# Kernel optimization log

Hardware: AMD Instinct MI355X
Metric: run time of the kernel (lower is better)

Reference implementation:

```python
import jax, jax.numpy as jnp
import numpy as np

VOCAB, EMBED, HIDDEN = 50000, 256, 512
BATCH, SEQ = 64, 512


def setup_inputs() -> dict:
    key = jax.random.key(0)
    ks = jax.random.split(key, 20)
    s = 0.05  # small init scale to keep gates out of saturation
    inp = {
        "tokens": jax.random.randint(ks[0], (BATCH, SEQ), 0, VOCAB, dtype=jnp.int64),
        "emb": jax.random.normal(ks[1], (VOCAB, EMBED), jnp.float32) * s,
        "W1f": jax.random.normal(ks[2], (EMBED, 4 * HIDDEN), jnp.float32) * s,
        "U1f": jax.random.normal(ks[3], (HIDDEN, 4 * HIDDEN), jnp.float32) * s,
        "b1f": jax.random.normal(ks[4], (4 * HIDDEN,), jnp.float32) * s,
        "W2f": jax.random.normal(ks[5], (HIDDEN, 4 * HIDDEN), jnp.float32) * s,
        "U2f": jax.random.normal(ks[6], (HIDDEN, 4 * HIDDEN), jnp.float32) * s,
        "b2f": jax.random.normal(ks[7], (4 * HIDDEN,), jnp.float32) * s,
        "W1b": jax.random.normal(ks[8], (EMBED, 4 * HIDDEN), jnp.float32) * s,
        "U1b": jax.random.normal(ks[9], (HIDDEN, 4 * HIDDEN), jnp.float32) * s,
        "b1b": jax.random.normal(ks[10], (4 * HIDDEN,), jnp.float32) * s,
        "W2b": jax.random.normal(ks[11], (HIDDEN, 4 * HIDDEN), jnp.float32) * s,
        "U2b": jax.random.normal(ks[12], (HIDDEN, 4 * HIDDEN), jnp.float32) * s,
        "b2b": jax.random.normal(ks[13], (4 * HIDDEN,), jnp.float32) * s,
        "Wd": jax.random.normal(ks[14], (2 * HIDDEN, 5), jnp.float32) * s,
        "bd": jax.random.normal(ks[15], (5,), jnp.float32) * s,
    }
    return inp


def _lstm_cell(x, h, c, W, U, b):
    # Keras gate order: i, f, g (candidate), o
    z = x @ W + h @ U + b
    i, f, g, o = jnp.split(z, 4, axis=-1)
    c = jax.nn.sigmoid(f) * c + jax.nn.sigmoid(i) * jnp.tanh(g)
    h = jax.nn.sigmoid(o) * jnp.tanh(c)
    return h, c


def _run_stack(xs, W1, U1, b1, W2, U2, b2):
    # xs: [T, B, E]; stacked 2-layer LSTM, return last hidden of layer 2: [B, H]
    B = xs.shape[1]
    H = U1.shape[0]
    init = tuple(jnp.zeros((B, H), xs.dtype) for _ in range(4))

    def step(carry, x_t):
        h1, c1, h2, c2 = carry
        h1, c1 = _lstm_cell(x_t, h1, c1, W1, U1, b1)
        h2, c2 = _lstm_cell(h1, h2, c2, W2, U2, b2)
        return (h1, c1, h2, c2), None

    (h1, c1, h2, c2), _ = jax.lax.scan(step, init, xs)
    return h2


def reference(tokens, emb, W1f, U1f, b1f, W2f, U2f, b2f,
              W1b, U1b, b1b, W2b, U2b, b2b, Wd, bd):
    x = emb[tokens]                 # [B, T, E]
    xs = jnp.swapaxes(x, 0, 1)      # [T, B, E]
    h_fwd = _run_stack(xs, W1f, U1f, b1f, W2f, U2f, b2f)          # [B, H]
    h_bwd = _run_stack(xs[::-1], W1b, U1b, b1b, W2b, U2b, b2b)    # [B, H]
    feat = jnp.concatenate([h_fwd, h_bwd], axis=-1)               # [B, 2H]
    return feat @ Wd + bd                                         # [B, 5]
```

## Files before the change

### kernel.cpp

```cpp
#include <hip/hip_runtime.h>
#include <hip/hip_bf16.h>

#define TSEQ 512
#define NB   64
#define NE   256
#define NH   512
#define NG   2048

static const size_t OFF_W1  = 0;
static const size_t OFF_W2  = 6291456;
static const size_t OFF_X   = 14680064;
static const size_t OFF_H1  = 31457280;
static const size_t OFF_H2  = 31981568;
static const size_t OFF_HF  = 32505856;
static const size_t OFF_CNT = 32636928;

typedef __bf16 v8bf __attribute__((ext_vector_type(8)));
typedef float  v4f  __attribute__((ext_vector_type(4)));

#define MFMA16(a_, b_, c_) __builtin_amdgcn_mfma_f32_16x16x32_bf16((a_), (b_), (c_), 0, 0, 0)

static __device__ __forceinline__ v8bf load_h8(const __bf16* p) {
    unsigned long long lo = __hip_atomic_load((unsigned long long*)p,     __ATOMIC_RELAXED, __HIP_MEMORY_SCOPE_AGENT);
    unsigned long long hi = __hip_atomic_load((unsigned long long*)p + 1, __ATOMIC_RELAXED, __HIP_MEMORY_SCOPE_AGENT);
    union { unsigned long long q[2]; v8bf v; } u;
    u.q[0] = lo; u.q[1] = hi;
    return u.v;
}

static __device__ __forceinline__ unsigned short bf16_bits(float f) {
    __bf16 b = (__bf16)f;
    return __builtin_bit_cast(unsigned short, b);
}

__global__ void wconv_kernel(const float* __restrict__ Wf, const float* __restrict__ Uf,
                             const float* __restrict__ Wb, const float* __restrict__ Ub,
                             char* __restrict__ dst, int NC, int KX)
{
    int id = blockIdx.x * 256 + threadIdx.x;
    int j    = id & 7;
    int lane = (id >> 3) & 63;
    int t    = (id >> 9) & 1;
    int rest = id >> 10;
    int c    = rest % NC;
    int ds   = rest / NC;
    int slice = ds & 63;
    int dirr  = ds >> 6;
    int coll = t * 16 + (lane & 15);
    int k    = c * 32 + (lane >> 4) * 8 + j;
    int gate = coll >> 3, jjj = coll & 7;
    int zcol = gate * 512 + slice * 8 + jjj;
    const float* W = dirr ? Wb : Wf;
    const float* U = dirr ? Ub : Uf;
    float v = (k < KX) ? W[(size_t)k * NG + zcol] : U[(size_t)(k - KX) * NG + zcol];
    ((__bf16*)dst)[id] = (__bf16)v;
}

__global__ void gather_x_kernel(const int* __restrict__ tokens, const float* __restrict__ emb,
                                char* __restrict__ ws)
{
    size_t id = (size_t)blockIdx.x * 256 + threadIdx.x;
    int j  = (int)(id & 7);
    int m  = (int)((id >> 3) & 63);
    int kb = (int)((id >> 9) & 31);
    int t  = (int)(id >> 14);
    int tok = tokens[m * TSEQ + t];
    float v = emb[(size_t)tok * NE + kb * 8 + j];
    ((__bf16*)(ws + OFF_X))[(size_t)t * 16384 + (kb * 64 + m) * 8 + j] = (__bf16)v;
    if (id < 16384) ((int*)(ws + OFF_CNT))[id] = 0;
}

template<int LAYER>
__device__ void run_layer(char* __restrict__ ws, const char* __restrict__ smem,
                          int dir, int slice, int tid,
                          const float* __restrict__ bb)
{
    const int lane = tid & 63;
    const int wv   = tid >> 6;
    const int colc = lane & 15;
    const int q    = lane >> 4;
    const int m0   = wv * 16;
    const int jj   = colc & 7;
    const int hcol = slice * 8 + jj;

    __bf16* h1ring = (__bf16*)(ws + OFF_H1 + (size_t)dir * (4 * 65536));
    __bf16* h2ring = (__bf16*)(ws + OFF_H2 + (size_t)dir * (4 * 65536));
    const char* Xfrag = ws + OFF_X;
    __bf16* hfin = (__bf16*)(ws + OFF_HF) + (size_t)dir * (NB * NH);

    int* T = (int*)(ws + OFF_CNT);
    const int rep = ((slice << 2) | wv) & 15;
    int* p1   = T + (dir * 2 + 0) * 4096 + rep * 256 + wv * 64 + lane;
    int* p2   = T + (dir * 2 + 1) * 4096 + rep * 256 + wv * 64 + lane;
    int* ownb = T + (dir * 2 + LAYER) * 4096;

    const float bi  = bb[hcol];
    const float bf_ = bb[512 + hcol];
    const float bg  = bb[1024 + hcol];
    const float bo  = bb[1536 + hcol];

    float cst[4] = {0.f, 0.f, 0.f, 0.f};

    const int aoff = (m0 + colc) * 8;

    #pragma unroll 1
    for (int s = 0; s < TSEQ; ++s) {
        v4f acc0a = {0,0,0,0}, acc1a = {0,0,0,0};
        v4f acc0b = {0,0,0,0}, acc1b = {0,0,0,0};

        if (LAYER == 0) {
            const int xs = dir ? (TSEQ - 1 - s) : s;
            const char* xb = Xfrag + (size_t)xs * 32768;
            #pragma unroll
            for (int c = 0; c < 8; ++c) {
                v8bf a  = *(const v8bf*)(xb + (((4 * c + q) * 64 + m0 + colc) * 16));
                v8bf w0 = *(const v8bf*)(smem + (c * 2 + 0) * 1024 + lane * 16);
                v8bf w1 = *(const v8bf*)(smem + (c * 2 + 1) * 1024 + lane * 16);
                if (c & 1) { acc0b = MFMA16(a, w0, acc0b); acc1b = MFMA16(a, w1, acc1b); }
                else       { acc0a = MFMA16(a, w0, acc0a); acc1a = MFMA16(a, w1, acc1a); }
            }
        }

        {
            const int t1 = LAYER ? s + 1 : s;
            const int t2 = LAYER ? s : s - 3;
            if (t1 > 0) {
                while (true) {
                    int v1 = __hip_atomic_load(p1, __ATOMIC_RELAXED, __HIP_MEMORY_SCOPE_AGENT);
                    bool ok = (v1 >= t1);
                    if (t2 > 0) {
                        int v2 = __hip_atomic_load(p2, __ATOMIC_RELAXED, __HIP_MEMORY_SCOPE_AGENT);
                        ok = ok && (v2 >= t2);
                    }
                    if (__all(ok)) break;
                }
            }
        }

        if (LAYER == 0) {
            if (s > 0) {
                const __bf16* hb = h1ring + (size_t)((s - 1) & 3) * 32768;
                v8bf ah[16];
                #pragma unroll
                for (int c = 0; c < 16; ++c)
                    ah[c] = load_h8(hb + (4 * c + q) * 512 + aoff);
                __builtin_amdgcn_sched_barrier(0);
                #pragma unroll
                for (int c = 0; c < 16; ++c) {
                    v8bf w0 = *(const v8bf*)(smem + ((8 + c) * 2 + 0) * 1024 + lane * 16);
                    v8bf w1 = *(const v8bf*)(smem + ((8 + c) * 2 + 1) * 1024 + lane * 16);
                    if (c & 1) { acc0b = MFMA16(ah[c], w0, acc0b); acc1b = MFMA16(ah[c], w1, acc1b); }
                    else       { acc0a = MFMA16(ah[c], w0, acc0a); acc1a = MFMA16(ah[c], w1, acc1a); }
                }
            }
        } else {
            const __bf16* hb1 = h1ring + (size_t)(s & 3) * 32768;
            v8bf a0[16], a1[16];
            #pragma unroll
            for (int c = 0; c < 16; ++c)
                a0[c] = load_h8(hb1 + (4 * c + q) * 512 + aoff);
            if (s > 0) {
                const __bf16* hb2 = h2ring + (size_t)((s - 1) & 3) * 32768;
                #pragma unroll
                for (int c = 0; c < 16; ++c)
                    a1[c] = load_h8(hb2 + (4 * c + q) * 512 + aoff);
            }
            __builtin_amdgcn_sched_barrier(0);
            #pragma unroll
            for (int c = 0; c < 16; ++c) {
                v8bf w0 = *(const v8bf*)(smem + (c * 2 + 0) * 1024 + lane * 16);
                v8bf w1 = *(const v8bf*)(smem + (c * 2 + 1) * 1024 + lane * 16);
                if (c & 1) { acc0b = MFMA16(a0[c], w0, acc0b); acc1b = MFMA16(a0[c], w1, acc1b); }
                else       { acc0a = MFMA16(a0[c], w0, acc0a); acc1a = MFMA16(a0[c], w1, acc1a); }
            }
            if (s > 0) {
                #pragma unroll
                for (int c = 0; c < 16; ++c) {
                    v8bf w0 = *(const v8bf*)(smem + ((16 + c) * 2 + 0) * 1024 + lane * 16);
                    v8bf w1 = *(const v8bf*)(smem + ((16 + c) * 2 + 1) * 1024 + lane * 16);
                    if (c & 1) { acc0b = MFMA16(a1[c], w0, acc0b); acc1b = MFMA16(a1[c], w1, acc1b); }
                    else       { acc0a = MFMA16(a1[c], w0, acc0a); acc1a = MFMA16(a1[c], w1, acc1a); }
                }
            }
        }

        v4f z0 = acc0a + acc0b;
        v4f z1 = acc1a + acc1b;

        float hv[4];
        #pragma unroll
        for (int r = 0; r < 4; ++r) {
            float p0 = __shfl_xor(z0[r], 8, 64);
            float p1 = __shfl_xor(z1[r], 8, 64);
            float zi, zf, zg, zo;
            if (colc < 8) { zi = z0[r]; zf = p0;    zg = z1[r]; zo = p1;    }
            else          { zi = p0;    zf = z0[r]; zg = p1;    zo = z1[r]; }
            zi += bi; zf += bf_; zg += bg; zo += bo;
            float gi = 1.f / (1.f + __expf(-zi));
            float gf = 1.f / (1.f + __expf(-zf));
            float gg = 1.f - 2.f / (1.f + __expf(2.f * zg));
            float go = 1.f / (1.f + __expf(-zo));
            float cn = gf * cst[r] + gi * gg;
            cst[r] = cn;
            float th = 1.f - 2.f / (1.f + __expf(2.f * cn));
            hv[r] = go * th;
        }

        __bf16* hd = (LAYER ? h2ring : h1ring) + (size_t)(s & 3) * 32768;
        {
            unsigned u0, u1, u2, u3;
            {
                float pv0 = __shfl_xor(hv[0], 1, 64);
                float pv1 = __shfl_xor(hv[1], 1, 64);
                float pv2 = __shfl_xor(hv[2], 1, 64);
                float pv3 = __shfl_xor(hv[3], 1, 64);
                u0 = (unsigned)bf16_bits(hv[0]) | ((unsigned)bf16_bits(pv0) << 16);
                u1 = (unsigned)bf16_bits(hv[1]) | ((unsigned)bf16_bits(pv1) << 16);
                u2 = (unsigned)bf16_bits(hv[2]) | ((unsigned)bf16_bits(pv2) << 16);
                u3 = (unsigned)bf16_bits(hv[3]) | ((unsigned)bf16_bits(pv3) << 16);
            }
            const bool sel1 = (colc & 2) != 0;
            const bool sel2 = (colc & 4) != 0;
            unsigned t;
            t = __shfl_xor(sel1 ? u0 : u1, 2, 64); if (sel1) u0 = t; else u1 = t;
            t = __shfl_xor(sel1 ? u2 : u3, 2, 64); if (sel1) u2 = t; else u3 = t;
            t = __shfl_xor(sel2 ? u0 : u2, 4, 64); if (sel2) u0 = t; else u2 = t;
            t = __shfl_xor(sel2 ? u1 : u3, 4, 64); if (sel2) u1 = t; else u3 = t;
            if (((colc & 1) == 0) && (colc < 8)) {
                const int m = m0 + q * 4 + (colc >> 1);
                unsigned long long lo = (unsigned long long)u0 | ((unsigned long long)u1 << 32);
                unsigned long long hi = (unsigned long long)u2 | ((unsigned long long)u3 << 32);
                unsigned long long* dp = (unsigned long long*)(hd + (slice * 64 + m) * 8);
                __hip_atomic_store(dp,     lo, __ATOMIC_RELAXED, __HIP_MEMORY_SCOPE_AGENT);
                __hip_atomic_store(dp + 1, hi, __ATOMIC_RELAXED, __HIP_MEMORY_SCOPE_AGENT);
            }
        }
        if (LAYER == 1 && s == TSEQ - 1 && colc < 8) {
            #pragma unroll
            for (int r = 0; r < 4; ++r)
                hfin[(size_t)(m0 + q * 4 + r) * NH + hcol] = (__bf16)hv[r];
        }

        asm volatile("s_waitcnt vmcnt(0)" ::: "memory");
        if (lane < 16)
            __hip_atomic_store(ownb + lane * 256 + wv * 64 + slice, s + 1,
                               __ATOMIC_RELAXED, __HIP_MEMORY_SCOPE_AGENT);
    }
}

__global__ __launch_bounds__(256, 1) void lstm_persist(
    char* __restrict__ ws,
    const float* __restrict__ b1f, const float* __restrict__ b2f,
    const float* __restrict__ b1b, const float* __restrict__ b2b)
{
    const int tid   = threadIdx.x;
    const int bid   = blockIdx.x;
    const int dir   = bid >> 7;
    const int layer = (bid >> 6) & 1;
    const int slice = bid & 63;

    const int NC = layer ? 32 : 24;
    const int wbytes = NC * 2048;

    __shared__ char smem[65536];
    {
        const char* wsrc = ws + (layer ? OFF_W2 : OFF_W1)
                         + (size_t)(dir * 64 + slice) * (size_t)wbytes;
        for (int i = tid * 16; i < wbytes; i += 256 * 16)
            *(uint4*)(smem + i) = *(const uint4*)(wsrc + i);
    }
    __syncthreads();

    const float* bb = layer ? (dir ? b2b : b2f) : (dir ? b1b : b1f);
    if (layer == 0) run_layer<0>(ws, smem, dir, slice, tid, bb);
    else            run_layer<1>(ws, smem, dir, slice, tid, bb);
}

__global__ void head_kernel(const char* __restrict__ ws, const float* __restrict__ Wd,
                            const float* __restrict__ bd, float* __restrict__ out)
{
    int b = blockIdx.x;
    int lane = threadIdx.x;
    const __bf16* hfF = (const __bf16*)(ws + OFF_HF) + (size_t)b * NH;
    const __bf16* hfB = (const __bf16*)(ws + OFF_HF) + (size_t)(NB * NH) + (size_t)b * NH;
    #pragma unroll
    for (int o = 0; o < 5; ++o) {
        float sum = 0.f;
        for (int k = lane; k < 2 * NH; k += 64) {
            float fv = (k < NH) ? (float)hfF[k] : (float)hfB[k - NH];
            sum += fv * Wd[(size_t)k * 5 + o];
        }
        #pragma unroll
        for (int off = 32; off > 0; off >>= 1) sum += __shfl_down(sum, off, 64);
        if (lane == 0) out[b * 5 + o] = sum + bd[o];
    }
}

extern "C" void kernel_launch(void* const* d_in, const int* in_sizes, int n_in,
                              void* d_out, int out_size, void* d_ws, size_t ws_size,
                              hipStream_t stream)
{
    const int*   tokens = (const int*)  d_in[0];
    const float* emb    = (const float*)d_in[1];
    const float* W1f    = (const float*)d_in[2];
    const float* U1f    = (const float*)d_in[3];
    const float* b1f    = (const float*)d_in[4];
    const float* W2f    = (const float*)d_in[5];
    const float* U2f    = (const float*)d_in[6];
    const float* b2f    = (const float*)d_in[7];
    const float* W1b    = (const float*)d_in[8];
    const float* U1b    = (const float*)d_in[9];
    const float* b1b    = (const float*)d_in[10];
    const float* W2b    = (const float*)d_in[11];
    const float* U2b    = (const float*)d_in[12];
    const float* b2b    = (const float*)d_in[13];
    const float* Wd     = (const float*)d_in[14];
    const float* bd     = (const float*)d_in[15];
    char* ws = (char*)d_ws;

    wconv_kernel<<<12288, 256, 0, stream>>>(W1f, U1f, W1b, U1b, ws + OFF_W1, 24, 256);
    wconv_kernel<<<16384, 256, 0, stream>>>(W2f, U2f, W2b, U2b, ws + OFF_W2, 32, 512);
    gather_x_kernel<<<32768, 256, 0, stream>>>(tokens, emb, ws);
    lstm_persist<<<256, 256, 0, stream>>>(ws, b1f, b2f, b1b, b2b);
    head_kernel<<<NB, 64, 0, stream>>>(ws, Wd, bd, (float*)d_out);
}
```

Measured before the change: 3.510 ms.

## Replace layer-1 ready counters with parity-tagged h data and speculative prefetch

Removes the per-step counter polling between producers and consumers of the h1/h2 rings. Each stored bf16 value now carries a parity bit (bit 14) that flips every four steps, and consumers re-load until every fragment shows the expected parity. h values are clamped so that bit is never set by real data. Next-step h fragments are issued right after the store so loads overlap the barrier latency, and only the layer-0 backpressure counter remains. This trades a small precision loss (one exponent bit repurposed, clamp to ±0.996) and possible repeated reloads for fewer atomic round trips on the serial critical path.

```diff
diff --git a/kernel.cpp b/kernel.cpp
--- a/kernel.cpp
+++ b/kernel.cpp
@@ -20,9 +20,12 @@
 
 #define MFMA16(a_, b_, c_) __builtin_amdgcn_mfma_f32_16x16x32_bf16((a_), (b_), (c_), 0, 0, 0)
 
+#define AG_LOAD(p)     __hip_atomic_load((p), __ATOMIC_RELAXED, __HIP_MEMORY_SCOPE_AGENT)
+#define AG_STORE(p, v) __hip_atomic_store((p), (v), __ATOMIC_RELAXED, __HIP_MEMORY_SCOPE_AGENT)
+
 static __device__ __forceinline__ v8bf load_h8(const __bf16* p) {
-    unsigned long long lo = __hip_atomic_load((unsigned long long*)p,     __ATOMIC_RELAXED, __HIP_MEMORY_SCOPE_AGENT);
-    unsigned long long hi = __hip_atomic_load((unsigned long long*)p + 1, __ATOMIC_RELAXED, __HIP_MEMORY_SCOPE_AGENT);
+    unsigned long long lo = AG_LOAD((unsigned long long*)p);
+    unsigned long long hi = AG_LOAD((unsigned long long*)p + 1);
     union { unsigned long long q[2]; v8bf v; } u;
     u.q[0] = lo; u.q[1] = hi;
     return u.v;
@@ -32,6 +35,39 @@
     __bf16 b = (__bf16)f;
     return __builtin_bit_cast(unsigned short, b);
 }
+
+static __device__ __forceinline__ unsigned frag_chk_clr(v8bf* f, unsigned pm) {
+    union { v8bf v; unsigned u[4]; } a; a.v = *f;
+    unsigned bad = ((a.u[0] ^ pm) | (a.u[1] ^ pm) | (a.u[2] ^ pm) | (a.u[3] ^ pm)) & 0x40004000u;
+    a.u[0] &= 0xBFFFBFFFu; a.u[1] &= 0xBFFFBFFFu;
+    a.u[2] &= 0xBFFFBFFFu; a.u[3] &= 0xBFFFBFFFu;
+    *f = a.v;
+    return bad;
+}
+
+#define ISSUE16(sp_, base_)                                                    \
+    {                                                                          \
+        const __bf16* _b = (base_);                                            \
+        _Pragma("unroll")                                                      \
+        for (int c = 0; c < 16; ++c)                                           \
+            sp_[c] = load_h8(_b + (4 * c + q) * 512 + aoff);                   \
+    }
+
+#define VALIDATE16(sp_, base_, pm_)                                            \
+    {                                                                          \
+        const __bf16* _b = (base_);                                            \
+        const unsigned _pm = (pm_);                                            \
+        while (true) {                                                         \
+            unsigned _bad = 0u;                                                \
+            _Pragma("unroll")                                                  \
+            for (int c = 0; c < 16; ++c) _bad |= frag_chk_clr(&sp_[c], _pm);   \
+            if (__all(_bad == 0u)) break;                                      \
+            _Pragma("unroll")                                                  \
+            for (int c = 0; c < 16; ++c)                                       \
+                sp_[c] = load_h8(_b + (4 * c + q) * 512 + aoff);               \
+            __builtin_amdgcn_sched_barrier(0);                                 \
+        }                                                                      \
+    }
 
 __global__ void wconv_kernel(const float* __restrict__ Wf, const float* __restrict__ Uf,
                              const float* __restrict__ Wb, const float* __restrict__ Ub,
@@ -67,7 +103,8 @@
     int tok = tokens[m * TSEQ + t];
     float v = emb[(size_t)tok * NE + kb * 8 + j];
     ((__bf16*)(ws + OFF_X))[(size_t)t * 16384 + (kb * 64 + m) * 8 + j] = (__bf16)v;
-    if (id < 16384) ((int*)(ws + OFF_CNT))[id] = 0;
+    if (id < 262144) ((unsigned*)(ws + OFF_H1))[id] = 0x40004000u;
+    if (id < 16384)  ((int*)(ws + OFF_CNT))[id] = 0;
 }
 
 template<int LAYER>
@@ -90,9 +127,8 @@
 
     int* T = (int*)(ws + OFF_CNT);
     const int rep = ((slice << 2) | wv) & 15;
-    int* p1   = T + (dir * 2 + 0) * 4096 + rep * 256 + wv * 64 + lane;
-    int* p2   = T + (dir * 2 + 1) * 4096 + rep * 256 + wv * 64 + lane;
-    int* ownb = T + (dir * 2 + LAYER) * 4096;
+    int* p2   = T + dir * 4096 + rep * 256 + wv * 64 + lane;
+    int* ownb = T + dir * 4096;
 
     const float bi  = bb[hcol];
     const float bf_ = bb[512 + hcol];
@@ -100,13 +136,22 @@
     const float bo  = bb[1536 + hcol];
 
     float cst[4] = {0.f, 0.f, 0.f, 0.f};
-
     const int aoff = (m0 + colc) * 8;
+
+    v8bf sp0[16];
+    v8bf sp1[16];
+
+    if (LAYER == 1) { ISSUE16(sp0, h1ring); }
 
     #pragma unroll 1
     for (int s = 0; s < TSEQ; ++s) {
+        const unsigned pmC = ((s >> 2) & 1)       ? 0x40004000u : 0u;
+        const unsigned pmP = (((s - 1) >> 2) & 1) ? 0x40004000u : 0u;
+
         v4f acc0a = {0,0,0,0}, acc1a = {0,0,0,0};
         v4f acc0b = {0,0,0,0}, acc1b = {0,0,0,0};
+
+        int gvG = (LAYER == 0 && s > 3) ? AG_LOAD(p2) : 0x7fffffff;
 
         if (LAYER == 0) {
             const int xs = dir ? (TSEQ - 1 - s) : s;
@@ -119,67 +164,36 @@
                 if (c & 1) { acc0b = MFMA16(a, w0, acc0b); acc1b = MFMA16(a, w1, acc1b); }
                 else       { acc0a = MFMA16(a, w0, acc0a); acc1a = MFMA16(a, w1, acc1a); }
             }
-        }
-
-        {
-            const int t1 = LAYER ? s + 1 : s;
-            const int t2 = LAYER ? s : s - 3;
-            if (t1 > 0) {
-                while (true) {
-                    int v1 = __hip_atomic_load(p1, __ATOMIC_RELAXED, __HIP_MEMORY_SCOPE_AGENT);
-                    bool ok = (v1 >= t1);
-                    if (t2 > 0) {
-                        int v2 = __hip_atomic_load(p2, __ATOMIC_RELAXED, __HIP_MEMORY_SCOPE_AGENT);
-                        ok = ok && (v2 >= t2);
-                    }
-                    if (__all(ok)) break;
-                }
-            }
-        }
-
-        if (LAYER == 0) {
             if (s > 0) {
-                const __bf16* hb = h1ring + (size_t)((s - 1) & 3) * 32768;
-                v8bf ah[16];
-                #pragma unroll
-                for (int c = 0; c < 16; ++c)
-                    ah[c] = load_h8(hb + (4 * c + q) * 512 + aoff);
+                VALIDATE16(sp0, h1ring + (size_t)((s - 1) & 3) * 32768, pmP);
                 __builtin_amdgcn_sched_barrier(0);
                 #pragma unroll
                 for (int c = 0; c < 16; ++c) {
                     v8bf w0 = *(const v8bf*)(smem + ((8 + c) * 2 + 0) * 1024 + lane * 16);
                     v8bf w1 = *(const v8bf*)(smem + ((8 + c) * 2 + 1) * 1024 + lane * 16);
-                    if (c & 1) { acc0b = MFMA16(ah[c], w0, acc0b); acc1b = MFMA16(ah[c], w1, acc1b); }
-                    else       { acc0a = MFMA16(ah[c], w0, acc0a); acc1a = MFMA16(ah[c], w1, acc1a); }
+                    if (c & 1) { acc0b = MFMA16(sp0[c], w0, acc0b); acc1b = MFMA16(sp0[c], w1, acc1b); }
+                    else       { acc0a = MFMA16(sp0[c], w0, acc0a); acc1a = MFMA16(sp0[c], w1, acc1a); }
                 }
             }
         } else {
-            const __bf16* hb1 = h1ring + (size_t)(s & 3) * 32768;
-            v8bf a0[16], a1[16];
-            #pragma unroll
-            for (int c = 0; c < 16; ++c)
-                a0[c] = load_h8(hb1 + (4 * c + q) * 512 + aoff);
-            if (s > 0) {
-                const __bf16* hb2 = h2ring + (size_t)((s - 1) & 3) * 32768;
-                #pragma unroll
-                for (int c = 0; c < 16; ++c)
-                    a1[c] = load_h8(hb2 + (4 * c + q) * 512 + aoff);
-            }
+            VALIDATE16(sp0, h1ring + (size_t)(s & 3) * 32768, pmC);
             __builtin_amdgcn_sched_barrier(0);
             #pragma unroll
             for (int c = 0; c < 16; ++c) {
                 v8bf w0 = *(const v8bf*)(smem + (c * 2 + 0) * 1024 + lane * 16);
                 v8bf w1 = *(const v8bf*)(smem + (c * 2 + 1) * 1024 + lane * 16);
-                if (c & 1) { acc0b = MFMA16(a0[c], w0, acc0b); acc1b = MFMA16(a0[c], w1, acc1b); }
-                else       { acc0a = MFMA16(a0[c], w0, acc0a); acc1a = MFMA16(a0[c], w1, acc1a); }
+                if (c & 1) { acc0b = MFMA16(sp0[c], w0, acc0b); acc1b = MFMA16(sp0[c], w1, acc1b); }
+                else       { acc0a = MFMA16(sp0[c], w0, acc0a); acc1a = MFMA16(sp0[c], w1, acc1a); }
             }
             if (s > 0) {
+                VALIDATE16(sp1, h2ring + (size_t)((s - 1) & 3) * 32768, pmP);
+                __builtin_amdgcn_sched_barrier(0);
                 #pragma unroll
                 for (int c = 0; c < 16; ++c) {
                     v8bf w0 = *(const v8bf*)(smem + ((16 + c) * 2 + 0) * 1024 + lane * 16);
                     v8bf w1 = *(const v8bf*)(smem + ((16 + c) * 2 + 1) * 1024 + lane * 16);
-                    if (c & 1) { acc0b = MFMA16(a1[c], w0, acc0b); acc1b = MFMA16(a1[c], w1, acc1b); }
-                    else       { acc0a = MFMA16(a1[c], w0, acc0a); acc1a = MFMA16(a1[c], w1, acc1a); }
+                    if (c & 1) { acc0b = MFMA16(sp1[c], w0, acc0b); acc1b = MFMA16(sp1[c], w1, acc1b); }
+                    else       { acc0a = MFMA16(sp1[c], w0, acc0a); acc1a = MFMA16(sp1[c], w1, acc1a); }
                 }
             }
         }
@@ -203,7 +217,14 @@
             float cn = gf * cst[r] + gi * gg;
             cst[r] = cn;
             float th = 1.f - 2.f / (1.f + __expf(2.f * cn));
-            hv[r] = go * th;
+            hv[r] = fminf(fmaxf(go * th, -0.99609375f), 0.99609375f);
+        }
+
+        if (LAYER == 0 && s > 3 && !__all(gvG >= s - 3)) {
+            while (true) {
+                int v2 = AG_LOAD(p2);
+                if (__all(v2 >= s - 3)) break;
+            }
         }
 
         __bf16* hd = (LAYER ? h2ring : h1ring) + (size_t)(s & 3) * 32768;
@@ -228,11 +249,12 @@
             t = __shfl_xor(sel2 ? u1 : u3, 4, 64); if (sel2) u1 = t; else u3 = t;
             if (((colc & 1) == 0) && (colc < 8)) {
                 const int m = m0 + q * 4 + (colc >> 1);
-                unsigned long long lo = (unsigned long long)u0 | ((unsigned long long)u1 << 32);
-                unsigned long long hi = (unsigned long long)u2 | ((unsigned long long)u3 << 32);
+                const unsigned long long pm64 = pmC ? 0x4000400040004000ULL : 0ULL;
+                unsigned long long lo = ((unsigned long long)u0 | ((unsigned long long)u1 << 32)) | pm64;
+                unsigned long long hi = ((unsigned long long)u2 | ((unsigned long long)u3 << 32)) | pm64;
                 unsigned long long* dp = (unsigned long long*)(hd + (slice * 64 + m) * 8);
-                __hip_atomic_store(dp,     lo, __ATOMIC_RELAXED, __HIP_MEMORY_SCOPE_AGENT);
-                __hip_atomic_store(dp + 1, hi, __ATOMIC_RELAXED, __HIP_MEMORY_SCOPE_AGENT);
+                AG_STORE(dp,     lo);
+                AG_STORE(dp + 1, hi);
             }
         }
         if (LAYER == 1 && s == TSEQ - 1 && colc < 8) {
@@ -241,10 +263,19 @@
                 hfin[(size_t)(m0 + q * 4 + r) * NH + hcol] = (__bf16)hv[r];
         }
 
-        asm volatile("s_waitcnt vmcnt(0)" ::: "memory");
-        if (lane < 16)
-            __hip_atomic_store(ownb + lane * 256 + wv * 64 + slice, s + 1,
-                               __ATOMIC_RELAXED, __HIP_MEMORY_SCOPE_AGENT);
+        if (LAYER == 1 && lane < 16)
+            AG_STORE(ownb + lane * 256 + wv * 64 + slice, s + 1);
+
+        __builtin_amdgcn_sched_barrier(0);
+        if (s < TSEQ - 1) {
+            if (LAYER == 0) {
+                ISSUE16(sp0, h1ring + (size_t)(s & 3) * 32768);
+            } else {
+                ISSUE16(sp0, h1ring + (size_t)((s + 1) & 3) * 32768);
+                ISSUE16(sp1, h2ring + (size_t)(s & 3) * 32768);
+            }
+        }
+        __builtin_amdgcn_sched_barrier(0);
     }
 }
 
```

Result: slower. 3.815 ms (+8.7%).
